# Kernel tuning notes

Measured on AMD Instinct MI355X. Metric: run time of the kernel, lower is better.

Reference implementation:

```python
import jax, jax.numpy as jnp
import numpy as np

H = 16        # num_attention_heads
D = 128       # head_dim
HID = 2048    # hidden_size
S = 2048      # seq_len
B = 2
EPS = 1.1920928955078125e-07  # torch.finfo(float32).eps, F.rms_norm default


def _rope(x, cos, sin):
    # x: [B,H,S,D]; cos/sin: [S, D//2] broadcast over B,H
    d = x.shape[-1] // 2
    x1, x2 = x[..., :d], x[..., d:]
    return jnp.concatenate([x1 * cos + x2 * sin, -x1 * sin + x2 * cos], axis=-1)


def _rmsnorm(x):
    ms = jnp.mean(x * x, axis=-1, keepdims=True)
    return x * jax.lax.rsqrt(ms + EPS)


def setup_inputs() -> dict:
    key = jax.random.key(0)
    ks = jax.random.split(key, 7)
    x = jax.random.normal(ks[0], (B, S, HID), dtype=jnp.float32)
    cos = jax.random.uniform(ks[1], (S, D // 2), dtype=jnp.float32)
    sin = jax.random.uniform(ks[2], (S, D // 2), dtype=jnp.float32)
    sc = 1.0 / np.sqrt(HID)
    wq = jax.random.normal(ks[3], (H * D, HID), dtype=jnp.float32) * sc
    wk = jax.random.normal(ks[4], (D, HID), dtype=jnp.float32) * sc  # num_kv_heads=1
    wv = jax.random.normal(ks[5], (D, HID), dtype=jnp.float32) * sc
    wo = jax.random.normal(ks[6], (HID, H * D), dtype=jnp.float32) * sc
    return {"x": x, "cos": cos, "sin": sin, "wq": wq, "wk": wk, "wv": wv, "wo": wo}


def reference(x, cos, sin, wq, wk, wv, wo):
    b, s, _ = x.shape
    # projections
    q = (x @ wq.T).reshape(b, s, H, D).transpose(0, 2, 1, 3)        # [b,H,s,D]
    k = (x @ wk.T).reshape(b, s, 1, D).transpose(0, 2, 1, 3)        # [b,1,s,D] MQA
    v = (x @ wv.T).reshape(b, s, 1, D).transpose(0, 2, 1, 3)
    # RoPE then RMS-norm on q/k (keep k/v in MQA [b,1,s,D]; broadcasting replaces expand)
    q = _rmsnorm(_rope(q, cos, sin))
    k = _rmsnorm(_rope(k, cos, sin))
    # causal attention
    scores = jnp.einsum('bhqd,bgkd->bhqk', q, k) * (D ** -0.5)      # [b,H,s,s]
    mask = jnp.tril(jnp.ones((s, s), dtype=bool))
    scores = jnp.where(mask, scores, -jnp.inf)
    attn = jax.nn.softmax(scores, axis=-1)
    out = jnp.einsum('bhqk,bgkd->bhqd', attn, v)                    # [b,H,s,D]
    out = out.transpose(0, 2, 1, 3).reshape(b, s, H * D)
    return out @ wo.T
```

## Files before the change

### kernel.cpp

```cpp
#include <hip/hip_runtime.h>
#include <hip/hip_bf16.h>

typedef __attribute__((ext_vector_type(8))) short bf16x8;
typedef __attribute__((ext_vector_type(4))) float f32x4;

constexpr int cH = 16, cD = 128, cHID = 2048, cS = 2048, cB = 2;
constexpr float cEPS = 1.1920928955078125e-07f;

__device__ __forceinline__ unsigned short f2bf(float f) {
  union { float f; unsigned u; } v; v.f = f;
  unsigned r = v.u + 0x7fffu + ((v.u >> 16) & 1u);
  return (unsigned short)(r >> 16);
}
__device__ __forceinline__ float bf2f(unsigned short h) {
  union { unsigned u; float f; } v; v.u = ((unsigned)h) << 16; return v.f;
}
__device__ __forceinline__ unsigned pk2(float a, float b) {
  return (unsigned)f2bf(a) | ((unsigned)f2bf(b) << 16);
}
__device__ __forceinline__ f32x4 mfma16(bf16x8 a, bf16x8 b, f32x4 c) {
  return __builtin_amdgcn_mfma_f32_16x16x32_bf16(a, b, c, 0, 0, 0);
}
__device__ __forceinline__ void gl2l(const void* g, void* l) {
  __builtin_amdgcn_global_load_lds(
      (const __attribute__((address_space(1))) unsigned int*)g,
      (__attribute__((address_space(3))) unsigned int*)l, 16, 0, 0);
}

__global__ __launch_bounds__(256) void cvt_qkv(
    const float* __restrict__ x, const float* __restrict__ wq,
    const float* __restrict__ wk, const float* __restrict__ wv,
    unsigned short* __restrict__ xb, unsigned short* __restrict__ wqb,
    unsigned short* __restrict__ wkb, unsigned short* __restrict__ wvb)
{
  long i = (long)blockIdx.x * 2048 + threadIdx.x * 8;
  const float* s; unsigned short* d; long off;
  if (i < 8388608)       { s = x;  d = xb;  off = i; }
  else if (i < 12582912) { s = wq; d = wqb; off = i - 8388608; }
  else if (i < 12845056) { s = wk; d = wkb; off = i - 12582912; }
  else                   { s = wv; d = wvb; off = i - 12845056; }
  float4 v0 = *reinterpret_cast<const float4*>(s + off);
  float4 v1 = *reinterpret_cast<const float4*>(s + off + 4);
  uint4 o; o.x = pk2(v0.x, v0.y); o.y = pk2(v0.z, v0.w);
  o.z = pk2(v1.x, v1.y); o.w = pk2(v1.z, v1.w);
  *reinterpret_cast<uint4*>(d + off) = o;
}

__global__ __launch_bounds__(256) void cvt_wo(
    const float* __restrict__ wo, unsigned short* __restrict__ wob)
{
  long i = (long)blockIdx.x * 2048 + threadIdx.x * 8;
  float4 v0 = *reinterpret_cast<const float4*>(wo + i);
  float4 v1 = *reinterpret_cast<const float4*>(wo + i + 4);
  uint4 o; o.x = pk2(v0.x, v0.y); o.y = pk2(v0.z, v0.w);
  o.z = pk2(v1.x, v1.y); o.w = pk2(v1.z, v1.w);
  *reinterpret_cast<uint4*>(wob + i) = o;
}

__global__ __launch_bounds__(256) void gemm_qkv(
    const unsigned short* __restrict__ A,
    const unsigned short* __restrict__ Wq,
    const unsigned short* __restrict__ Wk,
    const unsigned short* __restrict__ Wv,
    const float* __restrict__ cosb, const float* __restrict__ sinb,
    unsigned short* __restrict__ Qn,
    unsigned short* __restrict__ Kn,
    unsigned short* __restrict__ Vn)
{
  __shared__ unsigned short lds[17408];
  const int t = threadIdx.x;
  const int bm = blockIdx.x, bn = blockIdx.y;
  const int lane = t & 63, w = t >> 6;
  const int wr = w >> 1, wc = w & 1, hi = lane >> 4, l15 = lane & 15;

  const unsigned short* Wp; long wbase;
  if (bn < 16)       { Wp = Wq; wbase = (long)bn * 128; }
  else if (bn == 16) { Wp = Wk; wbase = 0; }
  else               { Wp = Wv; wbase = 0; }

  f32x4 acc[4][4] = {};

  for (int k0 = 0; k0 < 2048; k0 += 32) {
    #pragma unroll
    for (int i = 0; i < 2; ++i) {
      int c = w + 4 * i;
      gl2l(A + (long)(bm * 128 + 16 * c + (lane >> 2)) * 2048 + k0 + (lane & 3) * 8,
           &lds[c * 512]);
      gl2l(Wp + (wbase + 16 * c + (lane >> 2)) * 2048 + k0 + (lane & 3) * 8,
           &lds[4096 + c * 512]);
    }
    __syncthreads();
    bf16x8 af[4], bff[4];
    #pragma unroll
    for (int m = 0; m < 4; ++m)
      af[m] = *reinterpret_cast<const bf16x8*>(&lds[(wr * 64 + m * 16 + l15) * 32 + hi * 8]);
    #pragma unroll
    for (int n = 0; n < 4; ++n)
      bff[n] = *reinterpret_cast<const bf16x8*>(&lds[4096 + (wc * 64 + n * 16 + l15) * 32 + hi * 8]);
    #pragma unroll
    for (int m = 0; m < 4; ++m)
      #pragma unroll
      for (int n = 0; n < 4; ++n)
        acc[m][n] = mfma16(af[m], bff[n], acc[m][n]);
    __syncthreads();
  }

  #pragma unroll
  for (int m = 0; m < 4; ++m)
    #pragma unroll
    for (int n = 0; n < 4; ++n)
      #pragma unroll
      for (int r = 0; r < 4; ++r)
        lds[(wr * 64 + m * 16 + hi * 4 + r) * 136 + wc * 64 + n * 16 + l15] =
            f2bf(acc[m][n][r]);
  __syncthreads();

  const int r = t >> 1, h2 = t & 1;
  const int grow = bm * 128 + r, b = grow >> 11, s = grow & 2047;
  const unsigned short* Crow = &lds[r * 136];

  if (bn == 17) {
    long base = ((long)b * cS + s) * cD + h2 * 64;
    #pragma unroll
    for (int g = 0; g < 8; ++g) {
      const unsigned short* p = Crow + h2 * 64 + g * 8;
      uint4 o;
      o.x = (unsigned)p[0] | ((unsigned)p[1] << 16);
      o.y = (unsigned)p[2] | ((unsigned)p[3] << 16);
      o.z = (unsigned)p[4] | ((unsigned)p[5] << 16);
      o.w = (unsigned)p[6] | ((unsigned)p[7] << 16);
      *reinterpret_cast<uint4*>(&Vn[base + g * 8]) = o;
    }
  } else {
    float o1[32], o2[32];
    const float* cp = cosb + (long)s * 64 + h2 * 32;
    const float* sp = sinb + (long)s * 64 + h2 * 32;
    float ss = 0.f;
    #pragma unroll
    for (int j = 0; j < 32; ++j) {
      float x1 = bf2f(Crow[h2 * 32 + j]);
      float x2 = bf2f(Crow[64 + h2 * 32 + j]);
      float cv = cp[j], sv = sp[j];
      o1[j] = x1 * cv + x2 * sv;
      o2[j] = x2 * cv - x1 * sv;
      ss += o1[j] * o1[j] + o2[j] * o2[j];
    }
    ss += __shfl_xor(ss, 1);
    float scn = rsqrtf(ss * (1.0f / 128.0f) + cEPS);
    if (bn < 16) {
      long base = (((long)b * cH + bn) * cS + s) * cD + h2 * 32;
      #pragma unroll
      for (int g = 0; g < 4; ++g) {
        uint4 o;
        o.x = pk2(o1[g*8+0]*scn, o1[g*8+1]*scn); o.y = pk2(o1[g*8+2]*scn, o1[g*8+3]*scn);
        o.z = pk2(o1[g*8+4]*scn, o1[g*8+5]*scn); o.w = pk2(o1[g*8+6]*scn, o1[g*8+7]*scn);
        *reinterpret_cast<uint4*>(&Qn[base + g * 8]) = o;
      }
      #pragma unroll
      for (int g = 0; g < 4; ++g) {
        uint4 o;
        o.x = pk2(o2[g*8+0]*scn, o2[g*8+1]*scn); o.y = pk2(o2[g*8+2]*scn, o2[g*8+3]*scn);
        o.z = pk2(o2[g*8+4]*scn, o2[g*8+5]*scn); o.w = pk2(o2[g*8+6]*scn, o2[g*8+7]*scn);
        *reinterpret_cast<uint4*>(&Qn[base + 64 + g * 8]) = o;
      }
    } else {
      long base = ((long)b * cS + s) * cD;
      int xs = (s & 7) << 3;
      #pragma unroll
      for (int g = 0; g < 4; ++g) {
        int dlo = h2 * 32 + g * 8;
        uint4 o;
        o.x = pk2(o1[g*8+0]*scn, o1[g*8+1]*scn); o.y = pk2(o1[g*8+2]*scn, o1[g*8+3]*scn);
        o.z = pk2(o1[g*8+4]*scn, o1[g*8+5]*scn); o.w = pk2(o1[g*8+6]*scn, o1[g*8+7]*scn);
        *reinterpret_cast<uint4*>(&Kn[base + (dlo ^ xs)]) = o;
        uint4 p;
        p.x = pk2(o2[g*8+0]*scn, o2[g*8+1]*scn); p.y = pk2(o2[g*8+2]*scn, o2[g*8+3]*scn);
        p.z = pk2(o2[g*8+4]*scn, o2[g*8+5]*scn); p.w = pk2(o2[g*8+6]*scn, o2[g*8+7]*scn);
        *reinterpret_cast<uint4*>(&Kn[base + 64 + (dlo ^ xs)]) = p;
      }
    }
  }
}

__global__ __launch_bounds__(256) void vtrans(
    const unsigned short* __restrict__ Vn, unsigned short* __restrict__ Vt)
{
  __shared__ unsigned short Tl[64][72];
  const int t = threadIdx.x;
  const int st = blockIdx.x * 64, dt = blockIdx.y * 64, b = blockIdx.z;
  const unsigned short* Vb = Vn + (long)b * cS * cD;
  #pragma unroll
  for (int i = 0; i < 2; ++i) {
    int r = i * 32 + (t >> 3), c8 = (t & 7) * 8;
    *reinterpret_cast<uint4*>(&Tl[r][c8]) =
        *reinterpret_cast<const uint4*>(&Vb[(long)(st + r) * cD + dt + c8]);
  }
  __syncthreads();
  unsigned short* Vo = Vt + (long)b * cD * cS;
  #pragma unroll
  for (int i = 0; i < 2; ++i) {
    int d = i * 32 + (t >> 3), sb = (t & 7) * 8;
    unsigned short e[8];
    #pragma unroll
    for (int j = 0; j < 8; ++j) e[j] = Tl[sb + j][d];
    uint4 o;
    o.x = (unsigned)e[0] | ((unsigned)e[1] << 16);
    o.y = (unsigned)e[2] | ((unsigned)e[3] << 16);
    o.z = (unsigned)e[4] | ((unsigned)e[5] << 16);
    o.w = (unsigned)e[6] | ((unsigned)e[7] << 16);
    int dg = dt + d;
    *reinterpret_cast<uint4*>(&Vo[(long)dg * cS + st + (sb ^ ((dg & 7) << 3))]) = o;
  }
}

__global__ __launch_bounds__(256) void attn2(
    const unsigned short* __restrict__ Qn,
    const unsigned short* __restrict__ Kn,
    const unsigned short* __restrict__ Vt,
    unsigned short* __restrict__ O)
{
  __shared__ unsigned short lds[16384];
  const int t = threadIdx.x, w = t >> 6, lane = t & 63;
  const int hi = lane >> 4, l15 = lane & 15;
  const int h = blockIdx.y, b = blockIdx.z;
  const unsigned short* Qb = Qn + (long)(b * cH + h) * cS * cD;
  const unsigned short* Kb = Kn + (long)b * cS * cD;
  const unsigned short* Vtb = Vt + (long)b * cD * cS;
  const int x3 = (l15 & 7) << 3;
  const float sc2 = 0.08838834764831845f * 1.442695040888963f;

  #pragma unroll 1
  for (int pass = 0; pass < 2; ++pass) {
    const int qt = (pass == 0) ? blockIdx.x : 31 - blockIdx.x;
    const int q0 = qt * 64;
    const int qrow = q0 + w * 16 + l15;

    bf16x8 qf[4];
    #pragma unroll
    for (int kc = 0; kc < 4; ++kc)
      qf[kc] = *reinterpret_cast<const bf16x8*>(&Qb[(long)qrow * cD + kc * 32 + hi * 8]);

    f32x4 oacc[8] = {};
    float mrun = -1e30f, lrun = 0.f;
    const int nt = qt + 1;

    #pragma unroll 1
    for (int kt = 0; kt < nt; ++kt) {
      const int kv0 = kt * 64;
      __syncthreads();
      #pragma unroll
      for (int i = 0; i < 4; ++i) {
        int c = 4 * w + i;
        gl2l(Kb + (long)(kv0 + 4 * c + (lane >> 4)) * cD + (lane & 15) * 8,
             &lds[c * 512]);
        gl2l(Vtb + (long)(8 * c + (lane >> 3)) * cS + kv0 + (lane & 7) * 8,
             &lds[8192 + c * 512]);
      }
      __syncthreads();

      f32x4 st[4] = {};
      #pragma unroll
      for (int kc = 0; kc < 4; ++kc) {
        #pragma unroll
        for (int n = 0; n < 4; ++n) {
          bf16x8 kf = *reinterpret_cast<const bf16x8*>(
              &lds[(n * 16 + l15) * 128 + ((kc * 32 + hi * 8) ^ x3)]);
          st[n] = mfma16(kf, qf[kc], st[n]);
        }
      }

      float p[4][4];
      if (kt == qt) {
        #pragma unroll
        for (int n = 0; n < 4; ++n)
          #pragma unroll
          for (int r = 0; r < 4; ++r) {
            int kv = kv0 + n * 16 + hi * 4 + r;
            p[n][r] = (kv <= qrow) ? st[n][r] * sc2 : -1e30f;
          }
      } else {
        #pragma unroll
        for (int n = 0; n < 4; ++n)
          #pragma unroll
          for (int r = 0; r < 4; ++r)
            p[n][r] = st[n][r] * sc2;
      }

      float pmax = p[0][0];
      #pragma unroll
      for (int n = 0; n < 4; ++n)
        #pragma unroll
        for (int r = 0; r < 4; ++r) pmax = fmaxf(pmax, p[n][r]);
      pmax = fmaxf(pmax, __shfl_xor(pmax, 16));
      pmax = fmaxf(pmax, __shfl_xor(pmax, 32));
      float mnew = fmaxf(mrun, pmax);
      float alpha = exp2f(mrun - mnew);
      mrun = mnew;

      float psum = 0.f;
      #pragma unroll
      for (int n = 0; n < 4; ++n)
        #pragma unroll
        for (int r = 0; r < 4; ++r) {
          p[n][r] = exp2f(p[n][r] - mnew);
          psum += p[n][r];
        }
      psum += __shfl_xor(psum, 16);
      psum += __shfl_xor(psum, 32);
      lrun = lrun * alpha + psum;

      #pragma unroll
      for (int n = 0; n < 8; ++n)
        #pragma unroll
        for (int r = 0; r < 4; ++r) oacc[n][r] *= alpha;

      unsigned pkl[4], pkh[4];
      #pragma unroll
      for (int n = 0; n < 4; ++n) {
        pkl[n] = pk2(p[n][0], p[n][1]);
        pkh[n] = pk2(p[n][2], p[n][3]);
      }

      bf16x8 pa[2];
      #pragma unroll
      for (int c = 0; c < 2; ++c) {
        int ns = 2 * c + (hi >> 1);
        int no = 2 * c + ((hi >> 1) ^ 1);
        unsigned own0 = pkl[ns], own1 = pkh[ns];
        unsigned ot0 = pkl[no], ot1 = pkh[no];
        unsigned a160 = __shfl_xor(own0, 16), a161 = __shfl_xor(own1, 16);
        unsigned a320 = __shfl_xor(ot0, 32),  a321 = __shfl_xor(ot1, 32);
        unsigned a480 = __shfl_xor(ot0, 48),  a481 = __shfl_xor(ot1, 48);
        unsigned w0 = hi == 0 ? own0 : hi == 1 ? a480 : hi == 2 ? a320 : a160;
        unsigned w1 = hi == 0 ? own1 : hi == 1 ? a481 : hi == 2 ? a321 : a161;
        unsigned w2 = hi == 0 ? a160 : hi == 1 ? a320 : hi == 2 ? a480 : own0;
        unsigned w3 = hi == 0 ? a161 : hi == 1 ? a321 : hi == 2 ? a481 : own1;
        union { unsigned u[4]; bf16x8 v; } cvt;
        cvt.u[0] = w0; cvt.u[1] = w1; cvt.u[2] = w2; cvt.u[3] = w3;
        pa[c] = cvt.v;
      }

      #pragma unroll
      for (int n2 = 0; n2 < 8; ++n2) {
        #pragma unroll
        for (int c = 0; c < 2; ++c) {
          bf16x8 vf = *reinterpret_cast<const bf16x8*>(
              &lds[8192 + (n2 * 16 + l15) * 64 + ((c * 32 + hi * 8) ^ x3)]);
          oacc[n2] = mfma16(vf, pa[c], oacc[n2]);
        }
      }
    }

    __syncthreads();
    {
      float inv = 1.0f / lrun;
      unsigned short* Ol = &lds[w * 2176];
      #pragma unroll
      for (int n2 = 0; n2 < 8; ++n2)
        #pragma unroll
        for (int r = 0; r < 4; ++r)
          Ol[l15 * 136 + n2 * 16 + hi * 4 + r] = f2bf(oacc[n2][r] * inv);
      __syncthreads();
      #pragma unroll
      for (int i = 0; i < 4; ++i) {
        int row = hi + 4 * i;
        uint4 ov = *reinterpret_cast<const uint4*>(&Ol[row * 136 + l15 * 8]);
        *reinterpret_cast<uint4*>(
            &O[(long)(b * cS + q0 + w * 16 + row) * (cH * cD) + h * cD + l15 * 8]) = ov;
      }
    }
  }
}

__global__ __launch_bounds__(256) void gemm_out(
    const unsigned short* __restrict__ A,
    const unsigned short* __restrict__ W,
    float* __restrict__ C)
{
  __shared__ unsigned short lds[8192];
  const int t = threadIdx.x;
  const int bm = blockIdx.x, bn = blockIdx.y;
  const int lane = t & 63, w = t >> 6;
  const int wr = w >> 1, wc = w & 1, hi = lane >> 4, l15 = lane & 15;
  const long wbase = (long)bn * 128;

  f32x4 acc[4][4] = {};
  for (int k0 = 0; k0 < 2048; k0 += 32) {
    #pragma unroll
    for (int i = 0; i < 2; ++i) {
      int c = w + 4 * i;
      gl2l(A + (long)(bm * 128 + 16 * c + (lane >> 2)) * 2048 + k0 + (lane & 3) * 8,
           &lds[c * 512]);
      gl2l(W + (wbase + 16 * c + (lane >> 2)) * 2048 + k0 + (lane & 3) * 8,
           &lds[4096 + c * 512]);
    }
    __syncthreads();
    bf16x8 af[4], bff[4];
    #pragma unroll
    for (int m = 0; m < 4; ++m)
      af[m] = *reinterpret_cast<const bf16x8*>(&lds[(wr * 64 + m * 16 + l15) * 32 + hi * 8]);
    #pragma unroll
    for (int n = 0; n < 4; ++n)
      bff[n] = *reinterpret_cast<const bf16x8*>(&lds[4096 + (wc * 64 + n * 16 + l15) * 32 + hi * 8]);
    #pragma unroll
    for (int m = 0; m < 4; ++m)
      #pragma unroll
      for (int n = 0; n < 4; ++n)
        acc[m][n] = mfma16(af[m], bff[n], acc[m][n]);
    __syncthreads();
  }

  #pragma unroll
  for (int m = 0; m < 4; ++m) {
    int row = bm * 128 + wr * 64 + m * 16 + hi * 4;
    #pragma unroll
    for (int n = 0; n < 4; ++n) {
      int col = bn * 128 + wc * 64 + n * 16 + l15;
      #pragma unroll
      for (int r = 0; r < 4; ++r)
        C[(long)(row + r) * 2048 + col] = acc[m][n][r];
    }
  }
}

extern "C" void kernel_launch(void* const* d_in, const int* in_sizes, int n_in,
                              void* d_out, int out_size, void* d_ws, size_t ws_size,
                              hipStream_t stream) {
  const float* x    = (const float*)d_in[0];
  const float* cosb = (const float*)d_in[1];
  const float* sinb = (const float*)d_in[2];
  const float* wq   = (const float*)d_in[3];
  const float* wk   = (const float*)d_in[4];
  const float* wv   = (const float*)d_in[5];
  const float* wo   = (const float*)d_in[6];
  float* out = (float*)d_out;

  char* ws = (char*)d_ws;
  unsigned short* xb  = (unsigned short*)(ws);
  unsigned short* wqb = (unsigned short*)(ws + 16777216);
  unsigned short* wkb = (unsigned short*)(ws + 25165824);
  unsigned short* wvb = (unsigned short*)(ws + 25690112);
  unsigned short* Qn  = (unsigned short*)(ws + 26214400);
  unsigned short* Kn  = (unsigned short*)(ws + 42991616);
  unsigned short* Vn  = (unsigned short*)(ws + 44040192);
  unsigned short* Vtg = (unsigned short*)(ws + 45088768);
  unsigned short* Ob  = (unsigned short*)ws;
  unsigned short* wob = (unsigned short*)(ws + 16777216);

  cvt_qkv<<<dim3(6400), 256, 0, stream>>>(x, wq, wk, wv, xb, wqb, wkb, wvb);
  gemm_qkv<<<dim3(32, 18), 256, 0, stream>>>(xb, wqb, wkb, wvb, cosb, sinb, Qn, Kn, Vn);
  vtrans<<<dim3(32, 2, 2), 256, 0, stream>>>(Vn, Vtg);
  cvt_wo<<<dim3(2048), 256, 0, stream>>>(wo, wob);
  attn2<<<dim3(16, 16, 2), 256, 0, stream>>>(Qn, Kn, Vtg, Ob);
  gemm_out<<<dim3(32, 16), 256, 0, stream>>>(Ob, wob, out);
}
```

Baseline: 244.0 us.

## Give each wave full-head columns so RoPE/RMSnorm run from registers without LDS staging

Changes the QKV GEMM wave tiling from a 2x2 split (64x64 per wave) to 4x1 (32 rows x 128 columns per wave), so every wave holds a complete head-dim row in its accumulators. RoPE and RMS-norm are then applied directly from registers using cross-lane shuffles, and the LDS round-trip for the epilogue is removed along with its extra barrier. LDS allocation shrinks, which may allow higher occupancy. The trade-off is that each wave now reads all 8 B fragments per k-step (more LDS reads), and output is written as scattered 2-byte stores instead of 16-byte vector stores.

```diff
diff --git a/kernel.cpp b/kernel.cpp
--- a/kernel.cpp
+++ b/kernel.cpp
@@ -67,18 +67,18 @@
     unsigned short* __restrict__ Kn,
     unsigned short* __restrict__ Vn)
 {
-  __shared__ unsigned short lds[17408];
+  __shared__ unsigned short lds[8192];
   const int t = threadIdx.x;
   const int bm = blockIdx.x, bn = blockIdx.y;
   const int lane = t & 63, w = t >> 6;
-  const int wr = w >> 1, wc = w & 1, hi = lane >> 4, l15 = lane & 15;
+  const int hi = lane >> 4, l15 = lane & 15;
 
   const unsigned short* Wp; long wbase;
   if (bn < 16)       { Wp = Wq; wbase = (long)bn * 128; }
   else if (bn == 16) { Wp = Wk; wbase = 0; }
   else               { Wp = Wv; wbase = 0; }
 
-  f32x4 acc[4][4] = {};
+  f32x4 acc[2][8] = {};
 
   for (int k0 = 0; k0 < 2048; k0 += 32) {
     #pragma unroll
@@ -90,95 +90,71 @@
            &lds[4096 + c * 512]);
     }
     __syncthreads();
-    bf16x8 af[4], bff[4];
-    #pragma unroll
-    for (int m = 0; m < 4; ++m)
-      af[m] = *reinterpret_cast<const bf16x8*>(&lds[(wr * 64 + m * 16 + l15) * 32 + hi * 8]);
-    #pragma unroll
-    for (int n = 0; n < 4; ++n)
-      bff[n] = *reinterpret_cast<const bf16x8*>(&lds[4096 + (wc * 64 + n * 16 + l15) * 32 + hi * 8]);
-    #pragma unroll
-    for (int m = 0; m < 4; ++m)
-      #pragma unroll
-      for (int n = 0; n < 4; ++n)
+    bf16x8 af[2], bff[8];
+    #pragma unroll
+    for (int m = 0; m < 2; ++m)
+      af[m] = *reinterpret_cast<const bf16x8*>(&lds[(w * 32 + m * 16 + l15) * 32 + hi * 8]);
+    #pragma unroll
+    for (int n = 0; n < 8; ++n)
+      bff[n] = *reinterpret_cast<const bf16x8*>(&lds[4096 + (n * 16 + l15) * 32 + hi * 8]);
+    #pragma unroll
+    for (int m = 0; m < 2; ++m)
+      #pragma unroll
+      for (int n = 0; n < 8; ++n)
         acc[m][n] = mfma16(af[m], bff[n], acc[m][n]);
     __syncthreads();
   }
 
-  #pragma unroll
-  for (int m = 0; m < 4; ++m)
-    #pragma unroll
-    for (int n = 0; n < 4; ++n)
-      #pragma unroll
-      for (int r = 0; r < 4; ++r)
-        lds[(wr * 64 + m * 16 + hi * 4 + r) * 136 + wc * 64 + n * 16 + l15] =
-            f2bf(acc[m][n][r]);
-  __syncthreads();
-
-  const int r = t >> 1, h2 = t & 1;
-  const int grow = bm * 128 + r, b = grow >> 11, s = grow & 2047;
-  const unsigned short* Crow = &lds[r * 136];
-
+  const int rowbase = bm * 128 + w * 32;
   if (bn == 17) {
-    long base = ((long)b * cS + s) * cD + h2 * 64;
-    #pragma unroll
-    for (int g = 0; g < 8; ++g) {
-      const unsigned short* p = Crow + h2 * 64 + g * 8;
-      uint4 o;
-      o.x = (unsigned)p[0] | ((unsigned)p[1] << 16);
-      o.y = (unsigned)p[2] | ((unsigned)p[3] << 16);
-      o.z = (unsigned)p[4] | ((unsigned)p[5] << 16);
-      o.w = (unsigned)p[6] | ((unsigned)p[7] << 16);
-      *reinterpret_cast<uint4*>(&Vn[base + g * 8]) = o;
-    }
+    #pragma unroll
+    for (int m = 0; m < 2; ++m)
+      #pragma unroll
+      for (int r = 0; r < 4; ++r) {
+        int grow = rowbase + m * 16 + hi * 4 + r;
+        int b = grow >> 11, s = grow & 2047;
+        long base = ((long)b * cS + s) * cD;
+        #pragma unroll
+        for (int n = 0; n < 8; ++n)
+          Vn[base + n * 16 + l15] = f2bf(acc[m][n][r]);
+      }
   } else {
-    float o1[32], o2[32];
-    const float* cp = cosb + (long)s * 64 + h2 * 32;
-    const float* sp = sinb + (long)s * 64 + h2 * 32;
-    float ss = 0.f;
-    #pragma unroll
-    for (int j = 0; j < 32; ++j) {
-      float x1 = bf2f(Crow[h2 * 32 + j]);
-      float x2 = bf2f(Crow[64 + h2 * 32 + j]);
-      float cv = cp[j], sv = sp[j];
-      o1[j] = x1 * cv + x2 * sv;
-      o2[j] = x2 * cv - x1 * sv;
-      ss += o1[j] * o1[j] + o2[j] * o2[j];
-    }
-    ss += __shfl_xor(ss, 1);
-    float scn = rsqrtf(ss * (1.0f / 128.0f) + cEPS);
-    if (bn < 16) {
-      long base = (((long)b * cH + bn) * cS + s) * cD + h2 * 32;
-      #pragma unroll
-      for (int g = 0; g < 4; ++g) {
-        uint4 o;
-        o.x = pk2(o1[g*8+0]*scn, o1[g*8+1]*scn); o.y = pk2(o1[g*8+2]*scn, o1[g*8+3]*scn);
-        o.z = pk2(o1[g*8+4]*scn, o1[g*8+5]*scn); o.w = pk2(o1[g*8+6]*scn, o1[g*8+7]*scn);
-        *reinterpret_cast<uint4*>(&Qn[base + g * 8]) = o;
-      }
-      #pragma unroll
-      for (int g = 0; g < 4; ++g) {
-        uint4 o;
-        o.x = pk2(o2[g*8+0]*scn, o2[g*8+1]*scn); o.y = pk2(o2[g*8+2]*scn, o2[g*8+3]*scn);
-        o.z = pk2(o2[g*8+4]*scn, o2[g*8+5]*scn); o.w = pk2(o2[g*8+6]*scn, o2[g*8+7]*scn);
-        *reinterpret_cast<uint4*>(&Qn[base + 64 + g * 8]) = o;
-      }
-    } else {
-      long base = ((long)b * cS + s) * cD;
-      int xs = (s & 7) << 3;
-      #pragma unroll
-      for (int g = 0; g < 4; ++g) {
-        int dlo = h2 * 32 + g * 8;
-        uint4 o;
-        o.x = pk2(o1[g*8+0]*scn, o1[g*8+1]*scn); o.y = pk2(o1[g*8+2]*scn, o1[g*8+3]*scn);
-        o.z = pk2(o1[g*8+4]*scn, o1[g*8+5]*scn); o.w = pk2(o1[g*8+6]*scn, o1[g*8+7]*scn);
-        *reinterpret_cast<uint4*>(&Kn[base + (dlo ^ xs)]) = o;
-        uint4 p;
-        p.x = pk2(o2[g*8+0]*scn, o2[g*8+1]*scn); p.y = pk2(o2[g*8+2]*scn, o2[g*8+3]*scn);
-        p.z = pk2(o2[g*8+4]*scn, o2[g*8+5]*scn); p.w = pk2(o2[g*8+6]*scn, o2[g*8+7]*scn);
-        *reinterpret_cast<uint4*>(&Kn[base + 64 + (dlo ^ xs)]) = p;
-      }
-    }
+    #pragma unroll
+    for (int m = 0; m < 2; ++m)
+      #pragma unroll
+      for (int r = 0; r < 4; ++r) {
+        int grow = rowbase + m * 16 + hi * 4 + r;
+        int b = grow >> 11, s = grow & 2047;
+        float o1[4], o2[4], ss = 0.f;
+        #pragma unroll
+        for (int n = 0; n < 4; ++n) {
+          float cv = cosb[(long)s * 64 + n * 16 + l15];
+          float sv = sinb[(long)s * 64 + n * 16 + l15];
+          float x1 = acc[m][n][r], x2 = acc[m][n + 4][r];
+          o1[n] = x1 * cv + x2 * sv;
+          o2[n] = x2 * cv - x1 * sv;
+          ss += o1[n] * o1[n] + o2[n] * o2[n];
+        }
+        ss += __shfl_xor(ss, 1); ss += __shfl_xor(ss, 2);
+        ss += __shfl_xor(ss, 4); ss += __shfl_xor(ss, 8);
+        float scn = rsqrtf(ss * (1.0f / 128.0f) + cEPS);
+        if (bn < 16) {
+          long base = (((long)b * cH + bn) * cS + s) * cD;
+          #pragma unroll
+          for (int n = 0; n < 4; ++n) {
+            Qn[base + n * 16 + l15] = f2bf(o1[n] * scn);
+            Qn[base + 64 + n * 16 + l15] = f2bf(o2[n] * scn);
+          }
+        } else {
+          long base = ((long)b * cS + s) * cD;
+          int xs = (s & 7) << 3;
+          #pragma unroll
+          for (int n = 0; n < 4; ++n) {
+            Kn[base + ((n * 16 + l15) ^ xs)] = f2bf(o1[n] * scn);
+            Kn[base + (((64 + n * 16 + l15)) ^ xs)] = f2bf(o2[n] * scn);
+          }
+        }
+      }
   }
 }
 
```

After: 214.1 us. 1.14x faster.
